# Kernel tuning notes

Measured on AMD Instinct MI355X. Metric: run time of the kernel, lower is better.

Reference implementation:

```python
import jax, jax.numpy as jnp
import numpy as np

BETA = 1.0
TARGET_ENTROPY = 0.0
EPS = 1e-8


def setup_inputs() -> dict:
    key = jax.random.key(0)
    k1, k2 = jax.random.split(key)
    B, S, H, K = 4, 2048, 1024, 10
    hidden_states = jax.random.normal(k1, (B, S, H), dtype=jnp.float32)
    kernel_centers = jax.random.normal(k2, (K, H), dtype=jnp.float32) * 0.1
    kernel_weights = jnp.ones((K,), dtype=jnp.float32) / K
    kernel_scales = jnp.ones((K,), dtype=jnp.float32)  # kernel_bandwidth = 1.0
    return {
        "hidden_states": hidden_states,
        "kernel_centers": kernel_centers,
        "kernel_weights": kernel_weights,
        "kernel_scales": kernel_scales,
    }


def _knife_entropy(x, centers, weights, scales):
    # x: [N, H], centers: [K, H].  Gram-matrix form of sum_h (x-c)^2:
    x_sq = jnp.sum(x * x, axis=1, keepdims=True)          # [N, 1]
    c_sq = jnp.sum(centers * centers, axis=1)[None, :]    # [1, K]
    dist_sq = jnp.maximum(x_sq + c_sq - 2.0 * (x @ centers.T), 0.0)  # [N, K]
    kernel_vals = jnp.exp(-dist_sq / (2.0 * scales[None, :] ** 2))   # [N, K]
    density = kernel_vals @ weights                       # [N]
    return -jnp.mean(jnp.log(density + EPS))


def reference(hidden_states, kernel_centers, kernel_weights, kernel_scales):
    H = hidden_states.shape[-1]
    h_flat = hidden_states.reshape(-1, H)                 # [B*S, H]
    h_entropy = _knife_entropy(h_flat, kernel_centers, kernel_weights, kernel_scales)
    entropy_loss = BETA * h_entropy
    target_entropy_loss = (h_entropy - TARGET_ENTROPY) ** 2  # mse vs scalar target
    total_loss = entropy_loss + target_entropy_loss
    # order: entropy_loss, target_entropy_loss, total_loss, h_entropy
    return jnp.stack([entropy_loss, target_entropy_loss, total_loss, h_entropy])
```

## Files before the change

kernel.cpp:

```cpp
#include <hip/hip_runtime.h>
#include <math.h>

#define N_ROWS 8192
#define HDIM   1024
#define KK     10
#define EPSF   1e-8f

#define DPP_ADD(x, ctrl, rmask, bmask)                                        \
    x += __int_as_float(__builtin_amdgcn_update_dpp(                          \
        0, __float_as_int(x), ctrl, rmask, bmask, true))

__device__ __forceinline__ float wave_allreduce_add(float x) {
    DPP_ADD(x, 0x111, 0xf, 0xf);
    DPP_ADD(x, 0x112, 0xf, 0xf);
    DPP_ADD(x, 0x114, 0xf, 0xe);
    DPP_ADD(x, 0x118, 0xf, 0xc);
    DPP_ADD(x, 0x142, 0xa, 0xf);
    DPP_ADD(x, 0x143, 0xc, 0xf);
    return __int_as_float(__builtin_amdgcn_readlane(__float_as_int(x), 63));
}

__global__ __launch_bounds__(256, 2)
void knife_main(const float* __restrict__ x,
                const float* __restrict__ centers,
                const float* __restrict__ weights,
                const float* __restrict__ scales,
                float* __restrict__ partials) {
    const int lane = threadIdx.x & 63;
    const int wid  = threadIdx.x >> 6;
    const int gwave  = blockIdx.x * 4 + wid;
    const int nwaves = gridDim.x * 4;
    const int ROWS   = N_ROWS / 2048;

    const float4* c4 = (const float4*)centers;
    float4 c[KK][4];
#pragma unroll
    for (int k = 0; k < KK; ++k)
#pragma unroll
        for (int j = 0; j < 4; ++j)
            c[k][j] = c4[k * (HDIM / 4) + lane + 64 * j];

    float csq[KK];
#pragma unroll
    for (int k = 0; k < KK; ++k) {
        float s = 0.f;
#pragma unroll
        for (int j = 0; j < 4; ++j) {
            float4 v = c[k][j];
            s += v.x * v.x + v.y * v.y + v.z * v.z + v.w * v.w;
        }
        csq[k] = wave_allreduce_add(s);
    }

    float w[KK], inv2s2[KK];
#pragma unroll
    for (int k = 0; k < KK; ++k) {
        w[k] = weights[k];
        float sc = scales[k];
        inv2s2[k] = 1.0f / (2.0f * sc * sc);
    }

    const float4* x4 = (const float4*)x;
    float logsum = 0.f;

    int row = gwave;
    float4 xv[4], nx[4];
#pragma unroll
    for (int j = 0; j < 4; ++j)
        xv[j] = x4[((size_t)row << 8) + lane + 64 * j];

#pragma unroll
    for (int i = 0; i < 4; ++i) {
        const int nrow = row + nwaves;
        if (i + 1 < ROWS) {
#pragma unroll
            for (int j = 0; j < 4; ++j)
                nx[j] = x4[((size_t)nrow << 8) + lane + 64 * j];
        }

        float acc[KK + 1];
#pragma unroll
        for (int k = 0; k <= KK; ++k) acc[k] = 0.f;
#pragma unroll
        for (int j = 0; j < 4; ++j) {
            float4 v = xv[j];
            acc[KK] += v.x * v.x + v.y * v.y + v.z * v.z + v.w * v.w;
#pragma unroll
            for (int k = 0; k < KK; ++k) {
                float4 cv = c[k][j];
                acc[k] += v.x * cv.x + v.y * cv.y + v.z * cv.z + v.w * cv.w;
            }
        }

        float xsq = wave_allreduce_add(acc[KK]);
        float density = 0.f;
#pragma unroll
        for (int k = 0; k < KK; ++k) {
            float dot = wave_allreduce_add(acc[k]);
            float d = fmaxf(xsq + csq[k] - 2.0f * dot, 0.0f);
            density += w[k] * __expf(-d * inv2s2[k]);
        }
        logsum += __logf(density + EPSF);

#pragma unroll
        for (int j = 0; j < 4; ++j) xv[j] = nx[j];
        row = nrow;
    }

    __shared__ float red[4];
    if (lane == 0) red[wid] = logsum;
    __syncthreads();
    if (threadIdx.x == 0)
        partials[blockIdx.x] = red[0] + red[1] + red[2] + red[3];
}

__global__ __launch_bounds__(256)
void knife_final(const float* __restrict__ partials, float* __restrict__ out) {
    __shared__ float red[4];
    int t = threadIdx.x;
    float s = partials[t] + partials[t + 256];
    s = wave_allreduce_add(s);
    if ((t & 63) == 0) red[t >> 6] = s;
    __syncthreads();
    if (t == 0) {
        float total = red[0] + red[1] + red[2] + red[3];
        float h = -total / (float)N_ROWS;
        out[0] = h;
        out[1] = h * h;
        out[2] = h + h * h;
        out[3] = h;
    }
}

extern "C" void kernel_launch(void* const* d_in, const int* in_sizes, int n_in,
                              void* d_out, int out_size, void* d_ws, size_t ws_size,
                              hipStream_t stream) {
    const float* x       = (const float*)d_in[0];
    const float* centers = (const float*)d_in[1];
    const float* weights = (const float*)d_in[2];
    const float* scales  = (const float*)d_in[3];
    float* out      = (float*)d_out;
    float* partials = (float*)d_ws;

    knife_main<<<512, 256, 0, stream>>>(x, centers, weights, scales, partials);
    knife_final<<<1, 256, 0, stream>>>(partials, out);
}
```

Before: 86.98 us.

## Stage centers in LDS and load four contiguous rows per wave up front

The centers move from per-wave registers into a 40KB shared-memory tile loaded once per block. Each wave now owns four contiguous rows, all loaded at the start, and reuses each center fragment read from LDS across those four rows. Blocks become 512 threads with 256 blocks, which frees registers formerly holding centers and exposes all row loads at once for memory-level parallelism. In exchange it adds LDS traffic, a block-wide sync before compute, and drops the software prefetch pipeline.

```diff
diff --git a/kernel.cpp b/kernel.cpp
--- a/kernel.cpp
+++ b/kernel.cpp
@@ -5,6 +5,10 @@
 #define HDIM   1024
 #define KK     10
 #define EPSF   1e-8f
+#define NBLK   256
+#define TPB    512
+#define WPB    (TPB / 64)
+#define RPW    4
 
 #define DPP_ADD(x, ctrl, rmask, bmask)                                        \
     x += __int_as_float(__builtin_amdgcn_update_dpp(                          \
@@ -20,7 +24,7 @@
     return __int_as_float(__builtin_amdgcn_readlane(__float_as_int(x), 63));
 }
 
-__global__ __launch_bounds__(256, 2)
+__global__ __launch_bounds__(TPB, 2)
 void knife_main(const float* __restrict__ x,
                 const float* __restrict__ centers,
                 const float* __restrict__ weights,
@@ -28,29 +32,12 @@
                 float* __restrict__ partials) {
     const int lane = threadIdx.x & 63;
     const int wid  = threadIdx.x >> 6;
-    const int gwave  = blockIdx.x * 4 + wid;
-    const int nwaves = gridDim.x * 4;
-    const int ROWS   = N_ROWS / 2048;
+
+    __shared__ float4 cs[KK * (HDIM / 4)];
 
     const float4* c4 = (const float4*)centers;
-    float4 c[KK][4];
-#pragma unroll
-    for (int k = 0; k < KK; ++k)
-#pragma unroll
-        for (int j = 0; j < 4; ++j)
-            c[k][j] = c4[k * (HDIM / 4) + lane + 64 * j];
-
-    float csq[KK];
-#pragma unroll
-    for (int k = 0; k < KK; ++k) {
-        float s = 0.f;
-#pragma unroll
-        for (int j = 0; j < 4; ++j) {
-            float4 v = c[k][j];
-            s += v.x * v.x + v.y * v.y + v.z * v.z + v.w * v.w;
-        }
-        csq[k] = wave_allreduce_add(s);
-    }
+    for (int i = threadIdx.x; i < KK * (HDIM / 4); i += TPB)
+        cs[i] = c4[i];
 
     float w[KK], inv2s2[KK];
 #pragma unroll
@@ -60,65 +47,84 @@
         inv2s2[k] = 1.0f / (2.0f * sc * sc);
     }
 
-    const float4* x4 = (const float4*)x;
-    float logsum = 0.f;
+    const int g  = blockIdx.x * WPB + wid;
+    const int r0 = g * RPW;
+    const float4* xr = (const float4*)x + ((size_t)r0 << 8);
+    float4 xv[RPW][4];
+#pragma unroll
+    for (int r = 0; r < RPW; ++r)
+#pragma unroll
+        for (int j = 0; j < 4; ++j)
+            xv[r][j] = xr[(size_t)r * 256 + lane + 64 * j];
 
-    int row = gwave;
-    float4 xv[4], nx[4];
+    __syncthreads();
+
+    float csq[KK];
 #pragma unroll
-    for (int j = 0; j < 4; ++j)
-        xv[j] = x4[((size_t)row << 8) + lane + 64 * j];
+    for (int k = 0; k < KK; ++k) {
+        float s = 0.f;
+#pragma unroll
+        for (int j = 0; j < 4; ++j) {
+            float4 v = cs[k * 256 + lane + 64 * j];
+            s += v.x * v.x + v.y * v.y + v.z * v.z + v.w * v.w;
+        }
+        csq[k] = wave_allreduce_add(s);
+    }
+
+    float acc[RPW][KK + 1];
+#pragma unroll
+    for (int r = 0; r < RPW; ++r)
+#pragma unroll
+        for (int k = 0; k <= KK; ++k) acc[r][k] = 0.f;
 
 #pragma unroll
-    for (int i = 0; i < 4; ++i) {
-        const int nrow = row + nwaves;
-        if (i + 1 < ROWS) {
+    for (int j = 0; j < 4; ++j) {
 #pragma unroll
-            for (int j = 0; j < 4; ++j)
-                nx[j] = x4[((size_t)nrow << 8) + lane + 64 * j];
+        for (int r = 0; r < RPW; ++r) {
+            float4 v = xv[r][j];
+            acc[r][KK] += v.x * v.x + v.y * v.y + v.z * v.z + v.w * v.w;
         }
-
-        float acc[KK + 1];
 #pragma unroll
-        for (int k = 0; k <= KK; ++k) acc[k] = 0.f;
+        for (int k = 0; k < KK; ++k) {
+            float4 cv = cs[k * 256 + lane + 64 * j];
 #pragma unroll
-        for (int j = 0; j < 4; ++j) {
-            float4 v = xv[j];
-            acc[KK] += v.x * v.x + v.y * v.y + v.z * v.z + v.w * v.w;
-#pragma unroll
-            for (int k = 0; k < KK; ++k) {
-                float4 cv = c[k][j];
-                acc[k] += v.x * cv.x + v.y * cv.y + v.z * cv.z + v.w * cv.w;
+            for (int r = 0; r < RPW; ++r) {
+                float4 v = xv[r][j];
+                acc[r][k] += v.x * cv.x + v.y * cv.y + v.z * cv.z + v.w * cv.w;
             }
         }
+    }
 
-        float xsq = wave_allreduce_add(acc[KK]);
+    float logsum = 0.f;
+#pragma unroll
+    for (int r = 0; r < RPW; ++r) {
+        float xsq = wave_allreduce_add(acc[r][KK]);
         float density = 0.f;
 #pragma unroll
         for (int k = 0; k < KK; ++k) {
-            float dot = wave_allreduce_add(acc[k]);
+            float dot = wave_allreduce_add(acc[r][k]);
             float d = fmaxf(xsq + csq[k] - 2.0f * dot, 0.0f);
             density += w[k] * __expf(-d * inv2s2[k]);
         }
         logsum += __logf(density + EPSF);
-
-#pragma unroll
-        for (int j = 0; j < 4; ++j) xv[j] = nx[j];
-        row = nrow;
     }
 
-    __shared__ float red[4];
+    __shared__ float red[WPB];
     if (lane == 0) red[wid] = logsum;
     __syncthreads();
-    if (threadIdx.x == 0)
-        partials[blockIdx.x] = red[0] + red[1] + red[2] + red[3];
+    if (threadIdx.x == 0) {
+        float t = 0.f;
+#pragma unroll
+        for (int i = 0; i < WPB; ++i) t += red[i];
+        partials[blockIdx.x] = t;
+    }
 }
 
 __global__ __launch_bounds__(256)
 void knife_final(const float* __restrict__ partials, float* __restrict__ out) {
     __shared__ float red[4];
     int t = threadIdx.x;
-    float s = partials[t] + partials[t + 256];
+    float s = partials[t];
     s = wave_allreduce_add(s);
     if ((t & 63) == 0) red[t >> 6] = s;
     __syncthreads();
@@ -142,6 +148,6 @@
     float* out      = (float*)d_out;
     float* partials = (float*)d_ws;
 
-    knife_main<<<512, 256, 0, stream>>>(x, centers, weights, scales, partials);
+    knife_main<<<NBLK, TPB, 0, stream>>>(x, centers, weights, scales, partials);
     knife_final<<<1, 256, 0, stream>>>(partials, out);
 }
```

Measured after the change: 87.90 us, median of 2. About the same (+1.0%).
